# Kernel tuning notes

Hardware: AMD Instinct MI355X
Metric: run time of the kernel (lower is better)

Reference implementation:

```python
import jax, jax.numpy as jnp
import numpy as np

KERNEL = 3
PAD = KERNEL // 2


def setup_inputs() -> dict:
    key = jax.random.key(0)
    k1, k2, k3, k4 = jax.random.split(key, 4)
    B, Cin, Cout, D = 2, 32, 64, 64
    x = jax.random.normal(k1, (B, Cin, D, D, D), dtype=jnp.float32)
    mask = jax.random.randint(k2, (B, D, D, D), 0, 2).astype(jnp.bool_)
    fan_in = Cin * KERNEL ** 3
    bound = 1.0 / np.sqrt(fan_in)
    weight = jax.random.uniform(k3, (Cout, Cin, KERNEL, KERNEL, KERNEL),
                                dtype=jnp.float32, minval=-bound, maxval=bound)
    bias = jax.random.uniform(k4, (Cout,), dtype=jnp.float32, minval=-bound, maxval=bound)
    return {"x": x, "mask": mask, "weight": weight, "bias": bias}


def reference(x, mask, weight, bias):
    # Dense conv3d with 'same' padding, then zero out unoccupied voxels
    # (the CUDA warp kernel only computes occupied voxels; others are 0).
    out = jax.lax.conv_general_dilated(
        x, weight,
        window_strides=(1, 1, 1),
        padding=[(PAD, PAD)] * 3,
        dimension_numbers=("NCDHW", "OIDHW", "NCDHW"),
    )
    out = out + bias[None, :, None, None, None]
    return out * mask[:, None, :, :, :].astype(out.dtype)
```

## Files before the change

### kernel.cpp

```cpp
#include <hip/hip_runtime.h>
#include <stdint.h>


#define DD 64
#define CIN 32
#define COUT 64

typedef __bf16 bf16x8 __attribute__((ext_vector_type(8)));
typedef float f32x16 __attribute__((ext_vector_type(16)));

#define ROW_B_    1056u
#define OCT_B     6336u
#define SLAB_B    25344u
#define PLANE_OCT (66u * ROW_B_)
#define XT_BYTES  ((size_t)2 * 64 * 4 * 66 * ROW_B_)
#define WPK_U16   (27 * 2 * 2 * 64 * 8)
#define WPK_BYTES ((size_t)WPK_U16 * 2)
#define ZP_BYTES  ((size_t)SLAB_B)
#define WS_NEEDED (XT_BYTES + WPK_BYTES + ZP_BYTES)
#define CONV_LDS  (3 * 25344)

__device__ __forceinline__ uint16_t f2bf(float f) {
    uint32_t u = __builtin_bit_cast(uint32_t, f);
    u += 0x7fffu + ((u >> 16) & 1u);
    return (uint16_t)(u >> 16);
}

__device__ __forceinline__ void gll16(const void* g, void* l) {
    __builtin_amdgcn_global_load_lds(
        (__attribute__((address_space(1))) void*)g,
        (__attribute__((address_space(3))) void*)l, 16, 0, 0);
}

__global__ void pack_weights(const float* __restrict__ w, uint16_t* __restrict__ wpk,
                             uint4* __restrict__ zp) {
    int flat = blockIdx.x * 256 + threadIdx.x;
    if (flat < WPK_U16) {
        int j   = flat & 7;
        int l   = (flat >> 3) & 63;
        int ct  = (flat >> 9) & 1;
        int cb  = (flat >> 10) & 1;
        int k27 = flat >> 11;
        int co = ct * 32 + (l & 31);
        int ci = cb * 16 + ((l >> 5) * 8) + j;
        wpk[flat] = f2bf(w[(co * CIN + ci) * 27 + k27]);
    } else if (flat - WPK_U16 < (int)(ZP_BYTES / 16)) {
        zp[flat - WPK_U16] = make_uint4(0, 0, 0, 0);
    }
}

__global__ __launch_bounds__(256)
void transpose_x(const float* __restrict__ x, uint16_t* __restrict__ xt) {
    __shared__ uint16_t tile[4 * 66 * 8];
    const int yy = blockIdx.x, z = blockIdx.y, b = blockIdx.z;
    const int y = yy - 1;
    const int t = threadIdx.x;
    uint4* dst0 = (uint4*)(xt + ((((size_t)(b * DD + z)) * 4 + 0) * 66 + yy) * (ROW_B_ / 2));
    const size_t oct_stride4 = PLANE_OCT / 16;

    if (y < 0 || y >= DD) {
        for (int i = t; i < 264; i += 256)
            dst0[(i / 66) * oct_stride4 + (i % 66)] = make_uint4(0, 0, 0, 0);
        return;
    }
    const int ci = t >> 3;
    const int xs = (t & 7) * 8;
    const float* src = x + ((((size_t)b * CIN + ci) * DD + z) * DD + y) * DD + xs;
    float4 v0 = *(const float4*)src;
    float4 v1 = *(const float4*)(src + 4);
    float vals[8] = {v0.x, v0.y, v0.z, v0.w, v1.x, v1.y, v1.z, v1.w};
    const int oct = ci >> 3, j = ci & 7;
#pragma unroll
    for (int e = 0; e < 8; ++e)
        tile[(oct * 66 + (xs + e + 1)) * 8 + j] = f2bf(vals[e]);
    if (t < 64) {
        const int o2 = t >> 4, s2 = ((t >> 3) & 1) ? 65 : 0, j2 = t & 7;
        tile[(o2 * 66 + s2) * 8 + j2] = 0;
    }
    __syncthreads();
    const uint4* t4 = (const uint4*)tile;
    for (int i = t; i < 264; i += 256)
        dst0[(i / 66) * oct_stride4 + (i % 66)] = t4[i];
}

__global__ __launch_bounds__(256, 2)
void conv_mfma(const uint16_t* __restrict__ xt, const uint16_t* __restrict__ wpk,
               const uint16_t* __restrict__ zp,
               const int* __restrict__ mask, const float* __restrict__ bias,
               float* __restrict__ out) {
    extern __shared__ __align__(16) unsigned char lds[];
    const int yq = blockIdx.x, z = blockIdx.y, b = blockIdx.z;
    const int y0 = yq * 4;
    const int tid = threadIdx.x;
    const int lane = tid & 63;
    const int w = __builtin_amdgcn_readfirstlane(tid >> 6);
    const int ct    = w & 1;
    const int xtile = w >> 1;
    const int u = lane & 31;
    const int h = lane >> 5;
    const int xoff = xtile * 32;

    for (int r = w; r < 12; r += 4) {
        const int zr = r >> 2, oct = r & 3;
        const int zz = z - 1 + zr;
        const char* g = (zz >= 0 && zz < DD)
            ? (const char*)xt + ((((size_t)(b * DD + zz)) * 4 + oct) * 66 + y0) * ROW_B_
            : (const char*)zp + oct * OCT_B;
        const unsigned l = (unsigned)(zr * SLAB_B + oct * OCT_B);
#pragma unroll
        for (int c = 0; c < 6; ++c)
            gll16(g + c * 1024 + lane * 16, &lds[l + (unsigned)c * 1024u]);
        if (lane < 12) gll16(g + 6144 + lane * 16, &lds[l + 6144u]);
    }

    bf16x8 wfA[9], wfB[9];
#define LOAD_WF(DST, zr_, cb_)                                                     \
    _Pragma("unroll") for (int q = 0; q < 9; ++q)                                  \
        DST[q] = *(const bf16x8*)(wpk                                              \
            + (size_t)((((zr_) * 9 + q) * 2 + (cb_)) * 2 + ct) * 512 + lane * 8);

    LOAD_WF(wfA, 0, 0)
    __syncthreads();

    f32x16 acc[4] = {};

#define PHASE(zr_, cb_, WFC, WFN, pzr, pcb, DOPRE)                                 \
    {   const unsigned ob = (unsigned)((zr_) * SLAB_B + ((cb_) * 2 + h) * OCT_B)   \
                          + (unsigned)(xoff + u) * 16u;                            \
        if (DOPRE) { LOAD_WF(WFN, pzr, pcb) }                                      \
        _Pragma("unroll") for (int t = 0; t < 6; ++t) {                            \
            bf16x8 bf[3];                                                          \
            _Pragma("unroll") for (int kx = 0; kx < 3; ++kx)                       \
                bf[kx] = *(const bf16x8*)&lds[ob + (unsigned)t * ROW_B_ + kx * 16u];\
            _Pragma("unroll") for (int ly = 0; ly < 4; ++ly) {                     \
                const int ky = t - ly;                                             \
                if (ky >= 0 && ky < 3) {                                           \
                    _Pragma("unroll") for (int kx = 0; kx < 3; ++kx)               \
                        acc[ly] = __builtin_amdgcn_mfma_f32_32x32x16_bf16(         \
                            WFC[ky * 3 + kx], bf[kx], acc[ly], 0, 0, 0);           \
                }                                                                  \
            }                                                                      \
        }                                                                          \
    }

    PHASE(0, 0, wfA, wfB, 0, 1, 1)
    PHASE(0, 1, wfB, wfA, 1, 0, 1)
    PHASE(1, 0, wfA, wfB, 1, 1, 1)
    PHASE(1, 1, wfB, wfA, 2, 0, 1)
    PHASE(2, 0, wfA, wfB, 2, 1, 1)
    PHASE(2, 1, wfB, wfA, 0, 0, 0)
#undef PHASE
#undef LOAD_WF

    const size_t mb = (((size_t)b * DD + z) * DD + y0) * DD + xoff + u;
    float m[4];
#pragma unroll
    for (int ly = 0; ly < 4; ++ly) m[ly] = mask[mb + ly * DD] ? 1.0f : 0.0f;
#pragma unroll
    for (int r = 0; r < 16; ++r) {
        const int co = ct * 32 + (r & 3) + 8 * (r >> 2) + 4 * h;
        const float bs = bias[co];
        const size_t o = (((size_t)(b * COUT + co) * DD + z) * DD + y0) * DD + xoff + u;
#pragma unroll
        for (int ly = 0; ly < 4; ++ly)
            out[o + ly * DD] = (acc[ly][r] + bs) * m[ly];
    }
}

#define CI_BLK 16
__global__ __launch_bounds__(256, 2)
void sparse_conv3d_f32(const float* __restrict__ x,
                       const int* __restrict__ mask,
                       const float* __restrict__ weight,
                       const float* __restrict__ bias,
                       float* __restrict__ out) {
    __shared__ float lds[9 * CI_BLK * 66];
    const int y = blockIdx.x, z = blockIdx.y, b = blockIdx.z;
    const int lane = threadIdx.x & 63;
    const int wave = __builtin_amdgcn_readfirstlane(threadIdx.x >> 6);
    float acc[16];
#pragma unroll
    for (int j = 0; j < 16; ++j) acc[j] = 0.0f;
    const int co0 = wave * 16;
    const float* wbase = weight + (size_t)co0 * (CIN * 27);
    for (int cbl = 0; cbl < 2; ++cbl) {
        if (cbl) __syncthreads();
        for (int i = wave; i < 9 * CI_BLK; i += 4) {
            const int r = i >> 4, ci_l = i & 15;
            const int zz = z + (r / 3) - 1, yy = y + (r % 3) - 1;
            const int ci = cbl * CI_BLK + ci_l;
            float v = 0.0f;
            if (zz >= 0 && zz < DD && yy >= 0 && yy < DD)
                v = x[((((size_t)b * CIN + ci) * DD + zz) * DD + yy) * DD + lane];
            float* row = &lds[(size_t)i * 66];
            row[1 + lane] = v;
            if (lane == 0) { row[0] = 0.0f; row[65] = 0.0f; }
        }
        __syncthreads();
        for (int ci_l = 0; ci_l < CI_BLK; ++ci_l) {
            const int ci = cbl * CI_BLK + ci_l;
#pragma unroll
            for (int kz = 0; kz < 3; ++kz) {
#pragma unroll
                for (int ky = 0; ky < 3; ++ky) {
                    const int r = kz * 3 + ky;
                    const float* xrow = &lds[(size_t)(r * CI_BLK + ci_l) * 66 + lane];
                    const float xv0 = xrow[0], xv1 = xrow[1], xv2 = xrow[2];
                    const float* wp = wbase + ci * 27 + kz * 9 + ky * 3;
#pragma unroll
                    for (int j = 0; j < 16; ++j) {
                        acc[j] += wp[(size_t)j * (CIN * 27) + 0] * xv0
                                + wp[(size_t)j * (CIN * 27) + 1] * xv1
                                + wp[(size_t)j * (CIN * 27) + 2] * xv2;
                    }
                }
            }
        }
    }
    const float m = mask[(((size_t)b * DD + z) * DD + y) * DD + lane] ? 1.0f : 0.0f;
#pragma unroll
    for (int j = 0; j < 16; ++j) {
        const int co = co0 + j;
        out[((((size_t)b * COUT + co) * DD + z) * DD + y) * DD + lane] = (acc[j] + bias[co]) * m;
    }
}
#undef CI_BLK

extern "C" void kernel_launch(void* const* d_in, const int* in_sizes, int n_in,
                              void* d_out, int out_size, void* d_ws, size_t ws_size,
                              hipStream_t stream) {
    const float* x    = (const float*)d_in[0];
    const int*   mask = (const int*)d_in[1];
    const float* w    = (const float*)d_in[2];
    const float* bias = (const float*)d_in[3];
    float*       out  = (float*)d_out;

    if (ws_size < WS_NEEDED) {
        sparse_conv3d_f32<<<dim3(DD, DD, 2), 256, 0, stream>>>(x, mask, w, bias, out);
        return;
    }

    uint16_t* xt  = (uint16_t*)d_ws;
    uint16_t* wpk = (uint16_t*)((char*)d_ws + XT_BYTES);
    uint16_t* zp  = (uint16_t*)((char*)d_ws + XT_BYTES + WPK_BYTES);

    pack_weights<<<(WPK_U16 + (int)(ZP_BYTES / 16) + 255) / 256, 256, 0, stream>>>(w, wpk, (uint4*)zp);
    transpose_x<<<dim3(66, DD, 2), 256, 0, stream>>>(x, xt);
    conv_mfma<<<dim3(16, DD, 2), 256, CONV_LDS, stream>>>(xt, wpk, zp, mask, bias, out);
}
```

Baseline: 99.12 us.

## Split conv output rows across twice as many waves per block

Raises the conv block from 4 to 8 waves, and each wave now computes 2 output y-rows instead of 4. That halves the accumulator registers per wave and allows higher occupancy under launch bounds of (512,4). In exchange, each wave loads the full weight fragments for only half the MFMA work, which doubles the weight-load traffic per output. The weight prefetch is also moved before the address computation. The LDS tile loading loop is spread across 8 waves, so each wave issues fewer loads.

```diff
diff --git a/kernel.cpp b/kernel.cpp
--- a/kernel.cpp
+++ b/kernel.cpp
@@ -83,7 +83,7 @@
         dst0[(i / 66) * oct_stride4 + (i % 66)] = t4[i];
 }
 
-__global__ __launch_bounds__(256, 2)
+__global__ __launch_bounds__(512, 4)
 void conv_mfma(const uint16_t* __restrict__ xt, const uint16_t* __restrict__ wpk,
                const uint16_t* __restrict__ zp,
                const int* __restrict__ mask, const float* __restrict__ bias,
@@ -95,12 +95,13 @@
     const int lane = tid & 63;
     const int w = __builtin_amdgcn_readfirstlane(tid >> 6);
     const int ct    = w & 1;
-    const int xtile = w >> 1;
+    const int xtile = (w >> 1) & 1;
+    const int wy    = w >> 2;
     const int u = lane & 31;
     const int h = lane >> 5;
     const int xoff = xtile * 32;
 
-    for (int r = w; r < 12; r += 4) {
+    for (int r = w; r < 12; r += 8) {
         const int zr = r >> 2, oct = r & 3;
         const int zz = z - 1 + zr;
         const char* g = (zz >= 0 && zz < DD)
@@ -122,23 +123,24 @@
     LOAD_WF(wfA, 0, 0)
     __syncthreads();
 
-    f32x16 acc[4] = {};
+    f32x16 acc0 = {}, acc1 = {};
 
 #define PHASE(zr_, cb_, WFC, WFN, pzr, pcb, DOPRE)                                 \
-    {   const unsigned ob = (unsigned)((zr_) * SLAB_B + ((cb_) * 2 + h) * OCT_B)   \
+    {   if (DOPRE) { LOAD_WF(WFN, pzr, pcb) }                                      \
+        const unsigned ob = (unsigned)((zr_) * SLAB_B + ((cb_) * 2 + h) * OCT_B)   \
                           + (unsigned)(xoff + u) * 16u;                            \
-        if (DOPRE) { LOAD_WF(WFN, pzr, pcb) }                                      \
-        _Pragma("unroll") for (int t = 0; t < 6; ++t) {                            \
+        _Pragma("unroll") for (int t = 0; t < 4; ++t) {                            \
             bf16x8 bf[3];                                                          \
             _Pragma("unroll") for (int kx = 0; kx < 3; ++kx)                       \
-                bf[kx] = *(const bf16x8*)&lds[ob + (unsigned)t * ROW_B_ + kx * 16u];\
-            _Pragma("unroll") for (int ly = 0; ly < 4; ++ly) {                     \
-                const int ky = t - ly;                                             \
-                if (ky >= 0 && ky < 3) {                                           \
-                    _Pragma("unroll") for (int kx = 0; kx < 3; ++kx)               \
-                        acc[ly] = __builtin_amdgcn_mfma_f32_32x32x16_bf16(         \
-                            WFC[ky * 3 + kx], bf[kx], acc[ly], 0, 0, 0);           \
-                }                                                                  \
+                bf[kx] = *(const bf16x8*)&lds[ob + (unsigned)(2 * wy + t) * ROW_B_ \
+                                              + kx * 16u];                         \
+            _Pragma("unroll") for (int kx = 0; kx < 3; ++kx) {                     \
+                if (t <= 2)                                      \
+                    acc0 = __builtin_amdgcn_mfma_f32_32x32x16_bf16(                \
+                        WFC[t * 3 + kx], bf[kx], acc0, 0, 0, 0);                   \
+                if (t >= 1)                                      \
+                    acc1 = __builtin_amdgcn_mfma_f32_32x32x16_bf16(                \
+                        WFC[(t - 1) * 3 + kx], bf[kx], acc1, 0, 0, 0);             \
             }                                                                      \
         }                                                                          \
     }
@@ -152,18 +154,17 @@
 #undef PHASE
 #undef LOAD_WF
 
-    const size_t mb = (((size_t)b * DD + z) * DD + y0) * DD + xoff + u;
-    float m[4];
-#pragma unroll
-    for (int ly = 0; ly < 4; ++ly) m[ly] = mask[mb + ly * DD] ? 1.0f : 0.0f;
+    const int ya = y0 + 2 * wy;
+    const size_t mb = (((size_t)b * DD + z) * DD + ya) * DD + xoff + u;
+    const float m0 = mask[mb]      ? 1.0f : 0.0f;
+    const float m1 = mask[mb + DD] ? 1.0f : 0.0f;
 #pragma unroll
     for (int r = 0; r < 16; ++r) {
         const int co = ct * 32 + (r & 3) + 8 * (r >> 2) + 4 * h;
         const float bs = bias[co];
-        const size_t o = (((size_t)(b * COUT + co) * DD + z) * DD + y0) * DD + xoff + u;
-#pragma unroll
-        for (int ly = 0; ly < 4; ++ly)
-            out[o + ly * DD] = (acc[ly][r] + bs) * m[ly];
+        const size_t o = (((size_t)(b * COUT + co) * DD + z) * DD + ya) * DD + xoff + u;
+        out[o]      = (acc0[r] + bs) * m0;
+        out[o + DD] = (acc1[r] + bs) * m1;
     }
 }
 
@@ -246,5 +247,5 @@
 
     pack_weights<<<(WPK_U16 + (int)(ZP_BYTES / 16) + 255) / 256, 256, 0, stream>>>(w, wpk, (uint4*)zp);
     transpose_x<<<dim3(66, DD, 2), 256, 0, stream>>>(x, xt);
-    conv_mfma<<<dim3(16, DD, 2), 256, CONV_LDS, stream>>>(xt, wpk, zp, mask, bias, out);
-}
+    conv_mfma<<<dim3(16, DD, 2), 512, CONV_LDS, stream>>>(xt, wpk, zp, mask, bias, out);
+}
```

Result: faster. 89.69 us (-9.5%).
